# Optimization experiments

Hardware: AMD Instinct MI355X
Metric: run time of the kernel (lower is better)

The kernel has to match this reference:

```python
import jax, jax.numpy as jnp
import numpy as np

BATCH, IN_F, OUT_F = 4096, 1024, 1024


def setup_inputs() -> dict:
    key = jax.random.key(0)
    kx, kw = jax.random.split(key)
    x = jax.random.normal(kx, (BATCH, IN_F, 4), dtype=jnp.float32)
    weight = jax.random.normal(kw, (OUT_F, IN_F, 4), dtype=jnp.float32) * 0.01
    bias = jnp.zeros((OUT_F, 4), dtype=jnp.float32)
    return {"x": x, "weight": weight, "bias": bias}


def reference(x, weight, bias):
    # x: (batch, in, 4) quaternions; weight: (out, in, 4); bias: (out, 4)
    # Hamilton product broadcast over (batch, out, in) then summed over in ==
    # 16 signed real GEMMs contracting the `in` dimension.
    ar, ai, aj, ak = x[..., 0], x[..., 1], x[..., 2], x[..., 3]          # (b, i)
    br, bi, bj, bk = weight[..., 0], weight[..., 1], weight[..., 2], weight[..., 3]  # (o, i)

    mm = lambda a, w: jnp.einsum('bi,oi->bo', a, w)

    out_r = mm(ar, br) - mm(ai, bi) - mm(aj, bj) - mm(ak, bk)
    out_i = mm(ar, bi) + mm(ai, br) + mm(aj, bk) - mm(ak, bj)
    out_j = mm(ar, bj) - mm(ai, bk) + mm(aj, br) + mm(ak, bi)
    out_k = mm(ar, bk) + mm(ai, bj) - mm(aj, bi) + mm(ak, br)

    out = jnp.stack([out_r, out_i, out_j, out_k], axis=-1)  # (b, o, 4)
    return out + bias
```

## Files before the change

### kernel.cpp

```cpp
#include <hip/hip_runtime.h>


typedef __bf16 bf16x8 __attribute__((ext_vector_type(8)));
typedef float floatx4 __attribute__((ext_vector_type(4)));

constexpr int M = 4096;
constexpr int N = 4096;
constexpr int K = 4096;
constexpr int BM = 256, BN = 256, BK = 64;

constexpr int CVT_BLOCKS = (M * K / 8) / 256;
constexpr int EXP_BLOCKS = (1024 * 1024 / 2) / 256;

#define BARRIER() asm volatile("s_barrier" ::: "memory")
#define SB()      __builtin_amdgcn_sched_barrier(0)
#define LGKM0()   do { asm volatile("s_waitcnt lgkmcnt(0)"); SB(); } while (0)
#define LGKM4()   do { asm volatile("s_waitcnt lgkmcnt(4)"); SB(); } while (0)
#define LDS_OFF(p) ((unsigned)(uintptr_t)(__attribute__((address_space(3))) const void*)(p))

__global__ void prep_kernel(const float* __restrict__ x, const float* __restrict__ w,
                            __bf16* __restrict__ A, __bf16* __restrict__ Wb) {
    const int b = blockIdx.x;
    if (b < CVT_BLOCKS) {
        const size_t i = (size_t)b * 256 + threadIdx.x;
        const float4* xp = (const float4*)x;
        float4 a = xp[2 * i];
        float4 c = xp[2 * i + 1];
        bf16x8 v;
        v[0] = (__bf16)a.x; v[1] = (__bf16)a.y; v[2] = (__bf16)a.z; v[3] = (__bf16)a.w;
        v[4] = (__bf16)c.x; v[5] = (__bf16)c.y; v[6] = (__bf16)c.z; v[7] = (__bf16)c.w;
        *(bf16x8*)(A + 8 * i) = v;
    } else {
        const int idx = (b - CVT_BLOCKS) * 256 + threadIdx.x;
        const int o  = idx >> 9;
        const int ip = (idx & 511) * 2;
        float4 q0 = ((const float4*)w)[o * 1024 + ip];
        float4 q1 = ((const float4*)w)[o * 1024 + ip + 1];
        __bf16* base = Wb + (size_t)(o * 4) * K + ip * 4;
        bf16x8 r;
        r[0] = (__bf16)q0.x; r[1] = (__bf16)(-q0.y); r[2] = (__bf16)(-q0.z); r[3] = (__bf16)(-q0.w);
        r[4] = (__bf16)q1.x; r[5] = (__bf16)(-q1.y); r[6] = (__bf16)(-q1.z); r[7] = (__bf16)(-q1.w);
        *(bf16x8*)(base) = r;
        r[0] = (__bf16)q0.y; r[1] = (__bf16)q0.x; r[2] = (__bf16)q0.w; r[3] = (__bf16)(-q0.z);
        r[4] = (__bf16)q1.y; r[5] = (__bf16)q1.x; r[6] = (__bf16)q1.w; r[7] = (__bf16)(-q1.z);
        *(bf16x8*)(base + (size_t)K) = r;
        r[0] = (__bf16)q0.z; r[1] = (__bf16)(-q0.w); r[2] = (__bf16)q0.x; r[3] = (__bf16)q0.y;
        r[4] = (__bf16)q1.z; r[5] = (__bf16)(-q1.w); r[6] = (__bf16)q1.x; r[7] = (__bf16)q1.y;
        *(bf16x8*)(base + (size_t)2 * K) = r;
        r[0] = (__bf16)q0.w; r[1] = (__bf16)q0.z; r[2] = (__bf16)(-q0.y); r[3] = (__bf16)q0.x;
        r[4] = (__bf16)q1.w; r[5] = (__bf16)q1.z; r[6] = (__bf16)(-q1.y); r[7] = (__bf16)q1.x;
        *(bf16x8*)(base + (size_t)3 * K) = r;
    }
}

__device__ __forceinline__ void gload_lds16(const __bf16* g, __bf16* l) {
    __builtin_amdgcn_global_load_lds(
        (const __attribute__((address_space(1))) void*)g,
        (__attribute__((address_space(3))) void*)l, 16, 0, 0);
}

template <int OFF>
__device__ __forceinline__ bf16x8 dsrO(unsigned base) {
    bf16x8 r;
    asm volatile("ds_read_b128 %0, %1 offset:%c2" : "=v"(r) : "v"(base), "i"(OFF));
    return r;
}

__global__ __launch_bounds__(512, 2) void qgemm_kernel(const __bf16* __restrict__ A,
                                                       const __bf16* __restrict__ B,
                                                       const float* __restrict__ bias,
                                                       float* __restrict__ C) {
    __shared__ __bf16 As[3][BM][BK];
    __shared__ __bf16 Bs[2][BN][BK];

    const int tid  = threadIdx.x;
    const int wave = tid >> 6;
    const int lane = tid & 63;

    const int bid = blockIdx.x;
    const int xcd = bid & 7;
    const int q   = bid >> 3;
    const int tm  = (xcd >> 2) * 8 + (q & 7);
    const int tn  = (xcd & 3) * 4 + (q >> 3);
    const int bm  = tm * BM;
    const int bn  = tn * BN;

    const int wm = (wave >> 2) * 128;
    const int wn = (wave & 3) * 64;

    const int srow = wave * 16 + (lane >> 3);
    const int schk = ((lane & 7) ^ (lane >> 3)) * 8;
    const __bf16* agA = A + (size_t)(bm + srow) * K + schk;
    const __bf16* agB = B + (size_t)(bn + srow) * K + schk;

    auto issueA = [&](int buf, int h, int t) {
        const __bf16* g = agA + (size_t)h * 128 * K + t * BK;
        gload_lds16(g,                 &As[buf][h * 128 + wave * 16][0]);
        gload_lds16(g + (size_t)8 * K, &As[buf][h * 128 + wave * 16 + 8][0]);
    };
    auto issueB = [&](int buf, int h, int t) {
        const __bf16* g = agB + (size_t)h * 128 * K + t * BK;
        gload_lds16(g,                 &Bs[buf][h * 128 + wave * 16][0]);
        gload_lds16(g + (size_t)8 * K, &Bs[buf][h * 128 + wave * 16 + 8][0]);
    };

    const int fl  = lane & 15;
    const int fq  = lane >> 4;
    const int fx7 = fl & 7;
    const unsigned ebo0 = (unsigned)(((fq)     ^ fx7) * 16);
    const unsigned ebo1 = (unsigned)(((4 + fq) ^ fx7) * 16);
    const unsigned aR0  = LDS_OFF(&As[0][0][0]) + (unsigned)(wm + fl) * 128u + ebo0;
    const unsigned aR1  = LDS_OFF(&As[0][0][0]) + (unsigned)(wm + fl) * 128u + ebo1;
    const unsigned aR0b1 = aR0 + 32768u, aR1b1 = aR1 + 32768u;
    const unsigned aR0b2 = aR0 + 65536u, aR1b2 = aR1 + 65536u;
    const unsigned bR0  = LDS_OFF(&Bs[0][0][0]) + (unsigned)(wn + fl) * 128u + ebo0;
    const unsigned bR1  = LDS_OFF(&Bs[0][0][0]) + (unsigned)(wn + fl) * 128u + ebo1;
    const unsigned bR0b1 = bR0 + 32768u, bR1b1 = bR1 + 32768u;

    floatx4 acc[8][4] = {};
    bf16x8 x0, x1, x2, x3;
    bf16x8 y0, y1, y2, y3;
    bf16x8 w0, w1, w2, w3;
    bf16x8 z0, z1, z2, z3;
    bf16x8 s0, s1, s2, s3;
    bf16x8 c0, c1, c2, c3;
    bf16x8 d0, d1, d2, d3;
    bf16x8 n0, n1, n2, n3;

#define HALFK(i0, i1, AA, AB, F0, F1, F2, F3)                                     \
    acc[i0][0] = __builtin_amdgcn_mfma_f32_16x16x32_bf16(AA, F0, acc[i0][0], 0, 0, 0); \
    acc[i1][0] = __builtin_amdgcn_mfma_f32_16x16x32_bf16(AB, F0, acc[i1][0], 0, 0, 0); \
    acc[i0][1] = __builtin_amdgcn_mfma_f32_16x16x32_bf16(AA, F1, acc[i0][1], 0, 0, 0); \
    acc[i1][1] = __builtin_amdgcn_mfma_f32_16x16x32_bf16(AB, F1, acc[i1][1], 0, 0, 0); \
    acc[i0][2] = __builtin_amdgcn_mfma_f32_16x16x32_bf16(AA, F2, acc[i0][2], 0, 0, 0); \
    acc[i1][2] = __builtin_amdgcn_mfma_f32_16x16x32_bf16(AB, F2, acc[i1][2], 0, 0, 0); \
    acc[i0][3] = __builtin_amdgcn_mfma_f32_16x16x32_bf16(AA, F3, acc[i0][3], 0, 0, 0); \
    acc[i1][3] = __builtin_amdgcn_mfma_f32_16x16x32_bf16(AB, F3, acc[i1][3], 0, 0, 0)

#define TILE(T, A0c, A1c, A0n, A1n, B0c, B1c, B0x, DA, DB, ISSA, ISSB, MIDVM)     \
    do {                                                                          \
                      \
        if (ISSA) { issueA(DA, 0, (T) + 2); issueA(DA, 1, (T) + 2); }             \
        s0 = dsrO<0>(B1c); s1 = dsrO<2048>(B1c);                                  \
        s2 = dsrO<4096>(B1c); s3 = dsrO<6144>(B1c);                               \
        y0 = dsrO<4096>(A0c); y1 = dsrO<4096>(A1c);                               \
        y2 = dsrO<6144>(A0c); y3 = dsrO<6144>(A1c);                               \
        SB();                                                                     \
        __builtin_amdgcn_s_setprio(1);                                            \
        HALFK(0, 1, x0, x2, c0, c1, c2, c3);                                      \
        __builtin_amdgcn_s_setprio(0);                                            \
        LGKM4();                                       \
        __builtin_amdgcn_s_setprio(1);                                            \
        HALFK(0, 1, x1, x3, s0, s1, s2, s3);                                      \
        __builtin_amdgcn_s_setprio(0);                                            \
                     \
        w0 = dsrO<8192>(A0c); w1 = dsrO<8192>(A1c);                               \
        w2 = dsrO<10240>(A0c); w3 = dsrO<10240>(A1c);                             \
        SB();                                                                     \
        LGKM4();                                       \
        __builtin_amdgcn_s_setprio(1);                                            \
        HALFK(2, 3, y0, y2, c0, c1, c2, c3);                                      \
        HALFK(2, 3, y1, y3, s0, s1, s2, s3);                                      \
        __builtin_amdgcn_s_setprio(0);                                            \
        LGKM0();                                                      \
        asm volatile("s_waitcnt vmcnt(" #MIDVM ")");    \
        BARRIER();                                        \
        if (ISSB) { issueB(DB, 0, (T) + 2); issueB(DB, 1, (T) + 2); }             \
              \
        z0 = dsrO<12288>(A0c); z1 = dsrO<12288>(A1c);                             \
        z2 = dsrO<14336>(A0c); z3 = dsrO<14336>(A1c);                             \
        d0 = dsrO<0>(B0x); d1 = dsrO<2048>(B0x);                                  \
        d2 = dsrO<4096>(B0x); d3 = dsrO<6144>(B0x);                               \
        SB();                                                                     \
        __builtin_amdgcn_s_setprio(1);                                            \
        HALFK(4, 5, w0, w2, c0, c1, c2, c3);                                      \
        HALFK(4, 5, w1, w3, s0, s1, s2, s3);                                      \
        __builtin_amdgcn_s_setprio(0);                                            \
                                        \
        LGKM4();                                       \
        n0 = dsrO<0>(A0n); n1 = dsrO<0>(A1n);                                     \
        n2 = dsrO<2048>(A0n); n3 = dsrO<2048>(A1n);                               \
        SB();                                                                     \
        __builtin_amdgcn_s_setprio(1);                                            \
        HALFK(6, 7, z0, z2, c0, c1, c2, c3);                                      \
        HALFK(6, 7, z1, z3, s0, s1, s2, s3);                                      \
        __builtin_amdgcn_s_setprio(0);                                            \
        LGKM0();                          \
        BARRIER();                                               \
        x0 = n0; x1 = n1; x2 = n2; x3 = n3;                                       \
        c0 = d0; c1 = d1; c2 = d2; c3 = d3;                                       \
    } while (0)

    issueB(0, 0, 0); issueB(0, 1, 0);
    issueA(0, 0, 0); issueA(0, 1, 0);
    issueB(1, 0, 1); issueB(1, 1, 1);
    issueA(1, 0, 1); issueA(1, 1, 1);
    asm volatile("s_waitcnt vmcnt(0)");
    BARRIER();
    x0 = dsrO<0>(aR0);    x1 = dsrO<0>(aR1);
    x2 = dsrO<2048>(aR0); x3 = dsrO<2048>(aR1);
    c0 = dsrO<0>(bR0);    c1 = dsrO<2048>(bR0);
    c2 = dsrO<4096>(bR0); c3 = dsrO<6144>(bR0);
    LGKM0();

    for (int t = 0; t < 60; t += 6) {
        TILE(t + 0, aR0,   aR1,   aR0b1, aR1b1, bR0,   bR1,   bR0b1, 2, 0, true, true, 4);
        TILE(t + 1, aR0b1, aR1b1, aR0b2, aR1b2, bR0b1, bR1b1, bR0,   0, 1, true, true, 4);
        TILE(t + 2, aR0b2, aR1b2, aR0,   aR1,   bR0,   bR1,   bR0b1, 1, 0, true, true, 4);
        TILE(t + 3, aR0,   aR1,   aR0b1, aR1b1, bR0b1, bR1b1, bR0,   2, 1, true, true, 4);
        TILE(t + 4, aR0b1, aR1b1, aR0b2, aR1b2, bR0,   bR1,   bR0b1, 0, 0, true, true, 4);
        TILE(t + 5, aR0b2, aR1b2, aR0,   aR1,   bR0b1, bR1b1, bR0,   1, 1, true, true, 4);
    }
    TILE(60, aR0,   aR1,   aR0b1, aR1b1, bR0,   bR1,   bR0b1, 2, 0, true,  true,  4);
    TILE(61, aR0b1, aR1b1, aR0b2, aR1b2, bR0b1, bR1b1, bR0,   0, 1, true,  true,  4);
    TILE(62, aR0b2, aR1b2, aR0,   aR1,   bR0,   bR1,   bR0b1, 1, 0, false, false, 0);

    {
        s0 = dsrO<0>(bR1b1); s1 = dsrO<2048>(bR1b1);
        s2 = dsrO<4096>(bR1b1); s3 = dsrO<6144>(bR1b1);
        y0 = dsrO<4096>(aR0); y1 = dsrO<4096>(aR1);
        y2 = dsrO<6144>(aR0); y3 = dsrO<6144>(aR1);
        SB();
        __builtin_amdgcn_s_setprio(1);
        HALFK(0, 1, x0, x2, c0, c1, c2, c3);
        __builtin_amdgcn_s_setprio(0);
        LGKM4();
        __builtin_amdgcn_s_setprio(1);
        HALFK(0, 1, x1, x3, s0, s1, s2, s3);
        __builtin_amdgcn_s_setprio(0);
        w0 = dsrO<8192>(aR0); w1 = dsrO<8192>(aR1);
        w2 = dsrO<10240>(aR0); w3 = dsrO<10240>(aR1);
        SB();
        LGKM4();
        __builtin_amdgcn_s_setprio(1);
        HALFK(2, 3, y0, y2, c0, c1, c2, c3);
        HALFK(2, 3, y1, y3, s0, s1, s2, s3);
        __builtin_amdgcn_s_setprio(0);
        LGKM0();
        z0 = dsrO<12288>(aR0); z1 = dsrO<12288>(aR1);
        z2 = dsrO<14336>(aR0); z3 = dsrO<14336>(aR1);
        SB();
        __builtin_amdgcn_s_setprio(1);
        HALFK(4, 5, w0, w2, c0, c1, c2, c3);
        HALFK(4, 5, w1, w3, s0, s1, s2, s3);
        __builtin_amdgcn_s_setprio(0);
        LGKM0();
        __builtin_amdgcn_s_setprio(1);
        HALFK(6, 7, z0, z2, c0, c1, c2, c3);
        HALFK(6, 7, z1, z3, s0, s1, s2, s3);
        __builtin_amdgcn_s_setprio(0);
    }

#pragma unroll
    for (int mt = 0; mt < 8; ++mt) {
        const int row = bm + wm + mt * 16 + fq * 4;
#pragma unroll
        for (int nt = 0; nt < 4; ++nt) {
            const int col = bn + wn + nt * 16 + fl;
            const float bv = bias[col];
            float* cp = C + (size_t)row * N + col;
#pragma unroll
            for (int r = 0; r < 4; ++r)
                cp[(size_t)r * N] = acc[mt][nt][r] + bv;
        }
    }
#undef TILE
#undef HALFK
}

extern "C" void kernel_launch(void* const* d_in, const int* in_sizes, int n_in,
                              void* d_out, int out_size, void* d_ws, size_t ws_size,
                              hipStream_t stream) {
    const float* x    = (const float*)d_in[0];
    const float* w    = (const float*)d_in[1];
    const float* bias = (const float*)d_in[2];
    float* out = (float*)d_out;

    __bf16* Abf  = (__bf16*)d_ws;
    __bf16* Wbig = (__bf16*)((char*)d_ws + (size_t)M * K * 2);

    prep_kernel<<<CVT_BLOCKS + EXP_BLOCKS, 256, 0, stream>>>(x, w, Abf, Wbig);

    qgemm_kernel<<<256, 512, 0, stream>>>(Abf, Wbig, bias, out);
}
```

Before: 235.9 us.

## Fuse fp32-to-bf16 conversion of x into GEMM A-tile loading

The separate pass that converted x (64 MB fp32) to a bf16 buffer is removed. The GEMM now loads fp32 x with global_load_dwordx4 into registers, converts to bf16 and writes swizzled tiles to LDS with ds_write, interleaved into the existing pipeline. B fragments are also double-buffered in named registers instead of being copied at the end of each tile. This removes a 64 MB read plus 32 MB write and the reread of the bf16 A. In exchange the main loop gets more VGPR pressure, extra VALU conversion work and vmcnt waits that may stall the MFMA pipeline.

```diff
diff --git a/kernel.cpp b/kernel.cpp
--- a/kernel.cpp
+++ b/kernel.cpp
@@ -9,48 +9,36 @@
 constexpr int K = 4096;
 constexpr int BM = 256, BN = 256, BK = 64;
 
-constexpr int CVT_BLOCKS = (M * K / 8) / 256;
 constexpr int EXP_BLOCKS = (1024 * 1024 / 2) / 256;
 
 #define BARRIER() asm volatile("s_barrier" ::: "memory")
 #define SB()      __builtin_amdgcn_sched_barrier(0)
 #define LGKM0()   do { asm volatile("s_waitcnt lgkmcnt(0)"); SB(); } while (0)
 #define LGKM4()   do { asm volatile("s_waitcnt lgkmcnt(4)"); SB(); } while (0)
+#define LGKM8()   do { asm volatile("s_waitcnt lgkmcnt(8)"); SB(); } while (0)
+#define VM(n)     do { asm volatile("s_waitcnt vmcnt(" #n ")"); SB(); } while (0)
 #define LDS_OFF(p) ((unsigned)(uintptr_t)(__attribute__((address_space(3))) const void*)(p))
 
-__global__ void prep_kernel(const float* __restrict__ x, const float* __restrict__ w,
-                            __bf16* __restrict__ A, __bf16* __restrict__ Wb) {
-    const int b = blockIdx.x;
-    if (b < CVT_BLOCKS) {
-        const size_t i = (size_t)b * 256 + threadIdx.x;
-        const float4* xp = (const float4*)x;
-        float4 a = xp[2 * i];
-        float4 c = xp[2 * i + 1];
-        bf16x8 v;
-        v[0] = (__bf16)a.x; v[1] = (__bf16)a.y; v[2] = (__bf16)a.z; v[3] = (__bf16)a.w;
-        v[4] = (__bf16)c.x; v[5] = (__bf16)c.y; v[6] = (__bf16)c.z; v[7] = (__bf16)c.w;
-        *(bf16x8*)(A + 8 * i) = v;
-    } else {
-        const int idx = (b - CVT_BLOCKS) * 256 + threadIdx.x;
-        const int o  = idx >> 9;
-        const int ip = (idx & 511) * 2;
-        float4 q0 = ((const float4*)w)[o * 1024 + ip];
-        float4 q1 = ((const float4*)w)[o * 1024 + ip + 1];
-        __bf16* base = Wb + (size_t)(o * 4) * K + ip * 4;
-        bf16x8 r;
-        r[0] = (__bf16)q0.x; r[1] = (__bf16)(-q0.y); r[2] = (__bf16)(-q0.z); r[3] = (__bf16)(-q0.w);
-        r[4] = (__bf16)q1.x; r[5] = (__bf16)(-q1.y); r[6] = (__bf16)(-q1.z); r[7] = (__bf16)(-q1.w);
-        *(bf16x8*)(base) = r;
-        r[0] = (__bf16)q0.y; r[1] = (__bf16)q0.x; r[2] = (__bf16)q0.w; r[3] = (__bf16)(-q0.z);
-        r[4] = (__bf16)q1.y; r[5] = (__bf16)q1.x; r[6] = (__bf16)q1.w; r[7] = (__bf16)(-q1.z);
-        *(bf16x8*)(base + (size_t)K) = r;
-        r[0] = (__bf16)q0.z; r[1] = (__bf16)(-q0.w); r[2] = (__bf16)q0.x; r[3] = (__bf16)q0.y;
-        r[4] = (__bf16)q1.z; r[5] = (__bf16)(-q1.w); r[6] = (__bf16)q1.x; r[7] = (__bf16)q1.y;
-        *(bf16x8*)(base + (size_t)2 * K) = r;
-        r[0] = (__bf16)q0.w; r[1] = (__bf16)q0.z; r[2] = (__bf16)(-q0.y); r[3] = (__bf16)q0.x;
-        r[4] = (__bf16)q1.w; r[5] = (__bf16)q1.z; r[6] = (__bf16)(-q1.y); r[7] = (__bf16)q1.x;
-        *(bf16x8*)(base + (size_t)3 * K) = r;
-    }
+__global__ void prep_kernel(const float* __restrict__ w, __bf16* __restrict__ Wb) {
+    const int idx = blockIdx.x * 256 + threadIdx.x;
+    const int o  = idx >> 9;
+    const int ip = (idx & 511) * 2;
+    float4 q0 = ((const float4*)w)[o * 1024 + ip];
+    float4 q1 = ((const float4*)w)[o * 1024 + ip + 1];
+    __bf16* base = Wb + (size_t)(o * 4) * K + ip * 4;
+    bf16x8 r;
+    r[0] = (__bf16)q0.x; r[1] = (__bf16)(-q0.y); r[2] = (__bf16)(-q0.z); r[3] = (__bf16)(-q0.w);
+    r[4] = (__bf16)q1.x; r[5] = (__bf16)(-q1.y); r[6] = (__bf16)(-q1.z); r[7] = (__bf16)(-q1.w);
+    *(bf16x8*)(base) = r;
+    r[0] = (__bf16)q0.y; r[1] = (__bf16)q0.x; r[2] = (__bf16)q0.w; r[3] = (__bf16)(-q0.z);
+    r[4] = (__bf16)q1.y; r[5] = (__bf16)q1.x; r[6] = (__bf16)q1.w; r[7] = (__bf16)(-q1.z);
+    *(bf16x8*)(base + (size_t)K) = r;
+    r[0] = (__bf16)q0.z; r[1] = (__bf16)(-q0.w); r[2] = (__bf16)q0.x; r[3] = (__bf16)q0.y;
+    r[4] = (__bf16)q1.z; r[5] = (__bf16)(-q1.w); r[6] = (__bf16)q1.x; r[7] = (__bf16)q1.y;
+    *(bf16x8*)(base + (size_t)2 * K) = r;
+    r[0] = (__bf16)q0.w; r[1] = (__bf16)q0.z; r[2] = (__bf16)(-q0.y); r[3] = (__bf16)q0.x;
+    r[4] = (__bf16)q1.w; r[5] = (__bf16)q1.z; r[6] = (__bf16)(-q1.y); r[7] = (__bf16)q1.x;
+    *(bf16x8*)(base + (size_t)3 * K) = r;
 }
 
 __device__ __forceinline__ void gload_lds16(const __bf16* g, __bf16* l) {
@@ -59,14 +47,29 @@
         (__attribute__((address_space(3))) void*)l, 16, 0, 0);
 }
 
+__device__ __forceinline__ float4 gl4(const float* p) {
+    float4 r;
+    asm volatile("global_load_dwordx4 %0, %1, off" : "=v"(r) : "v"(p));
+    return r;
+}
 template <int OFF>
 __device__ __forceinline__ bf16x8 dsrO(unsigned base) {
     bf16x8 r;
     asm volatile("ds_read_b128 %0, %1 offset:%c2" : "=v"(r) : "v"(base), "i"(OFF));
     return r;
 }
-
-__global__ __launch_bounds__(512, 2) void qgemm_kernel(const __bf16* __restrict__ A,
+template <int OFF>
+__device__ __forceinline__ void dswO(unsigned base, bf16x8 v) {
+    asm volatile("ds_write_b128 %0, %1 offset:%c2" :: "v"(base), "v"(v), "i"(OFF));
+}
+__device__ __forceinline__ bf16x8 cvt8(float4 a, float4 b) {
+    bf16x8 v;
+    v[0] = (__bf16)a.x; v[1] = (__bf16)a.y; v[2] = (__bf16)a.z; v[3] = (__bf16)a.w;
+    v[4] = (__bf16)b.x; v[5] = (__bf16)b.y; v[6] = (__bf16)b.z; v[7] = (__bf16)b.w;
+    return v;
+}
+
+__global__ __launch_bounds__(512, 2) void qgemm_kernel(const float* __restrict__ X,
                                                        const __bf16* __restrict__ B,
                                                        const float* __restrict__ bias,
                                                        float* __restrict__ C) {
@@ -88,21 +91,20 @@
     const int wm = (wave >> 2) * 128;
     const int wn = (wave & 3) * 64;
 
+    const float* agX = X + (size_t)(bm + wave * 16 + (lane >> 3)) * 4096 + (lane & 7) * 8;
     const int srow = wave * 16 + (lane >> 3);
     const int schk = ((lane & 7) ^ (lane >> 3)) * 8;
-    const __bf16* agA = A + (size_t)(bm + srow) * K + schk;
     const __bf16* agB = B + (size_t)(bn + srow) * K + schk;
 
-    auto issueA = [&](int buf, int h, int t) {
-        const __bf16* g = agA + (size_t)h * 128 * K + t * BK;
-        gload_lds16(g,                 &As[buf][h * 128 + wave * 16][0]);
-        gload_lds16(g + (size_t)8 * K, &As[buf][h * 128 + wave * 16 + 8][0]);
-    };
     auto issueB = [&](int buf, int h, int t) {
         const __bf16* g = agB + (size_t)h * 128 * K + t * BK;
         gload_lds16(g,                 &Bs[buf][h * 128 + wave * 16][0]);
         gload_lds16(g + (size_t)8 * K, &Bs[buf][h * 128 + wave * 16 + 8][0]);
     };
+
+    const unsigned aW0 = LDS_OFF(&As[0][0][0]) + (unsigned)((wave * 16 + (lane >> 3)) * 128)
+                       + (unsigned)(((lane & 7) ^ (lane >> 3)) * 16);
+    const unsigned aW1 = aW0 + 32768u, aW2 = aW0 + 65536u;
 
     const int fl  = lane & 15;
     const int fq  = lane >> 4;
@@ -118,14 +120,12 @@
     const unsigned bR0b1 = bR0 + 32768u, bR1b1 = bR1 + 32768u;
 
     floatx4 acc[8][4] = {};
-    bf16x8 x0, x1, x2, x3;
-    bf16x8 y0, y1, y2, y3;
-    bf16x8 w0, w1, w2, w3;
-    bf16x8 z0, z1, z2, z3;
+    bf16x8 xa0, xa1, xa2, xa3;
+    bf16x8 xb0, xb1, xb2, xb3;
     bf16x8 s0, s1, s2, s3;
-    bf16x8 c0, c1, c2, c3;
-    bf16x8 d0, d1, d2, d3;
-    bf16x8 n0, n1, n2, n3;
+    bf16x8 bE0, bE1, bE2, bE3;
+    bf16x8 bO0, bO1, bO2, bO3;
+    float4 fa0, fa1, fa2, fa3;
 
 #define HALFK(i0, i1, AA, AB, F0, F1, F2, F3)                                     \
     acc[i0][0] = __builtin_amdgcn_mfma_f32_16x16x32_bf16(AA, F0, acc[i0][0], 0, 0, 0); \
@@ -137,117 +137,161 @@
     acc[i0][3] = __builtin_amdgcn_mfma_f32_16x16x32_bf16(AA, F3, acc[i0][3], 0, 0, 0); \
     acc[i1][3] = __builtin_amdgcn_mfma_f32_16x16x32_bf16(AB, F3, acc[i1][3], 0, 0, 0)
 
-#define TILE(T, A0c, A1c, A0n, A1n, B0c, B1c, B0x, DA, DB, ISSA, ISSB, MIDVM)     \
+#define TILE(T, A0c, A1c, A0n, A1n, B0c, B1c, B0x, AW, BC0, BC1, BC2, BC3,        \
+             BX0, BX1, BX2, BX3, DB, ISSA, ISSB, MIDVM)                           \
     do {                                                                          \
-                      \
-        if (ISSA) { issueA(DA, 0, (T) + 2); issueA(DA, 1, (T) + 2); }             \
+                                                                          \
+        if (ISSA) {                                                               \
+            const float* g_ = agX + (size_t)((T) + 2) * 64;                       \
+            fa0 = gl4(g_);          fa1 = gl4(g_ + 4);                            \
+            fa2 = gl4(g_ + 32768);  fa3 = gl4(g_ + 32772);                        \
+        }                                                                         \
         s0 = dsrO<0>(B1c); s1 = dsrO<2048>(B1c);                                  \
         s2 = dsrO<4096>(B1c); s3 = dsrO<6144>(B1c);                               \
-        y0 = dsrO<4096>(A0c); y1 = dsrO<4096>(A1c);                               \
-        y2 = dsrO<6144>(A0c); y3 = dsrO<6144>(A1c);                               \
+        xb0 = dsrO<4096>(A0c); xb1 = dsrO<4096>(A1c);                             \
+        xb2 = dsrO<6144>(A0c); xb3 = dsrO<6144>(A1c);                             \
         SB();                                                                     \
         __builtin_amdgcn_s_setprio(1);                                            \
-        HALFK(0, 1, x0, x2, c0, c1, c2, c3);                                      \
-        __builtin_amdgcn_s_setprio(0);                                            \
-        LGKM4();                                       \
-        __builtin_amdgcn_s_setprio(1);                                            \
-        HALFK(0, 1, x1, x3, s0, s1, s2, s3);                                      \
-        __builtin_amdgcn_s_setprio(0);                                            \
-                     \
-        w0 = dsrO<8192>(A0c); w1 = dsrO<8192>(A1c);                               \
-        w2 = dsrO<10240>(A0c); w3 = dsrO<10240>(A1c);                             \
+        HALFK(0, 1, xa0, xa2, BC0, BC1, BC2, BC3);                                \
+        __builtin_amdgcn_s_setprio(0);                                            \
+        LGKM4();                                                                  \
+        __builtin_amdgcn_s_setprio(1);                                            \
+        HALFK(0, 1, xa1, xa3, s0, s1, s2, s3);                                    \
+        __builtin_amdgcn_s_setprio(0);                                            \
+                                                                          \
+        xa0 = dsrO<8192>(A0c); xa1 = dsrO<8192>(A1c);                             \
+        xa2 = dsrO<10240>(A0c); xa3 = dsrO<10240>(A1c);                           \
         SB();                                                                     \
-        LGKM4();                                       \
-        __builtin_amdgcn_s_setprio(1);                                            \
-        HALFK(2, 3, y0, y2, c0, c1, c2, c3);                                      \
-        HALFK(2, 3, y1, y3, s0, s1, s2, s3);                                      \
-        __builtin_amdgcn_s_setprio(0);                                            \
-        LGKM0();                                                      \
-        asm volatile("s_waitcnt vmcnt(" #MIDVM ")");    \
-        BARRIER();                                        \
+        LGKM4();                                                                  \
+        __builtin_amdgcn_s_setprio(1);                                            \
+        HALFK(2, 3, xb0, xb2, BC0, BC1, BC2, BC3);                                \
+        HALFK(2, 3, xb1, xb3, s0, s1, s2, s3);                                    \
+        __builtin_amdgcn_s_setprio(0);                                            \
+        LGKM0();                                                                  \
+        asm volatile("s_waitcnt vmcnt(" #MIDVM ")");                              \
+        BARRIER();                                                                \
+                                                                          \
+        if (ISSA) {                                                               \
+            VM(0);                           \
+            dswO<0>(AW, cvt8(fa0, fa1));                                          \
+            dswO<1024>(AW, cvt8(fa2, fa3));                                       \
+            const float* g_ = agX + (size_t)((T) + 2) * 64 + 524288;              \
+            fa0 = gl4(g_);          fa1 = gl4(g_ + 4);                            \
+            fa2 = gl4(g_ + 32768);  fa3 = gl4(g_ + 32772);                        \
+        }                                                                         \
         if (ISSB) { issueB(DB, 0, (T) + 2); issueB(DB, 1, (T) + 2); }             \
-              \
-        z0 = dsrO<12288>(A0c); z1 = dsrO<12288>(A1c);                             \
-        z2 = dsrO<14336>(A0c); z3 = dsrO<14336>(A1c);                             \
-        d0 = dsrO<0>(B0x); d1 = dsrO<2048>(B0x);                                  \
-        d2 = dsrO<4096>(B0x); d3 = dsrO<6144>(B0x);                               \
+        xb0 = dsrO<12288>(A0c); xb1 = dsrO<12288>(A1c);                           \
+        xb2 = dsrO<14336>(A0c); xb3 = dsrO<14336>(A1c);                           \
+        BX0 = dsrO<0>(B0x); BX1 = dsrO<2048>(B0x);                                \
+        BX2 = dsrO<4096>(B0x); BX3 = dsrO<6144>(B0x);                             \
         SB();                                                                     \
         __builtin_amdgcn_s_setprio(1);                                            \
-        HALFK(4, 5, w0, w2, c0, c1, c2, c3);                                      \
-        HALFK(4, 5, w1, w3, s0, s1, s2, s3);                                      \
-        __builtin_amdgcn_s_setprio(0);                                            \
-                                        \
-        LGKM4();                                       \
-        n0 = dsrO<0>(A0n); n1 = dsrO<0>(A1n);                                     \
-        n2 = dsrO<2048>(A0n); n3 = dsrO<2048>(A1n);                               \
+        HALFK(4, 5, xa0, xa2, BC0, BC1, BC2, BC3);                                \
+        HALFK(4, 5, xa1, xa3, s0, s1, s2, s3);                                    \
+        __builtin_amdgcn_s_setprio(0);                                            \
+                                                                          \
+        xa0 = dsrO<0>(A0n); xa1 = dsrO<0>(A1n);                                   \
+        xa2 = dsrO<2048>(A0n); xa3 = dsrO<2048>(A1n);                             \
         SB();                                                                     \
-        __builtin_amdgcn_s_setprio(1);                                            \
-        HALFK(6, 7, z0, z2, c0, c1, c2, c3);                                      \
-        HALFK(6, 7, z1, z3, s0, s1, s2, s3);                                      \
-        __builtin_amdgcn_s_setprio(0);                                            \
-        LGKM0();                          \
-        BARRIER();                                               \
-        x0 = n0; x1 = n1; x2 = n2; x3 = n3;                                       \
-        c0 = d0; c1 = d1; c2 = d2; c3 = d3;                                       \
+        LGKM8();                                     \
+        __builtin_amdgcn_s_setprio(1);                                            \
+        HALFK(6, 7, xb0, xb2, BC0, BC1, BC2, BC3);                                \
+        __builtin_amdgcn_s_setprio(0);                                            \
+        if (ISSA) {                                                               \
+            VM(4);                         \
+            dswO<16384>(AW, cvt8(fa0, fa1));                                      \
+            dswO<17408>(AW, cvt8(fa2, fa3));                                      \
+        }                                                                         \
+        __builtin_amdgcn_s_setprio(1);                                            \
+        HALFK(6, 7, xb1, xb3, s0, s1, s2, s3);                                    \
+        __builtin_amdgcn_s_setprio(0);                                            \
+        LGKM0();                                                                  \
+        BARRIER();                                                                \
     } while (0)
 
+    {
+        const float* g_ = agX;
+        fa0 = gl4(g_); fa1 = gl4(g_ + 4); fa2 = gl4(g_ + 32768); fa3 = gl4(g_ + 32772);
+        VM(0);
+        dswO<0>(aW0, cvt8(fa0, fa1)); dswO<1024>(aW0, cvt8(fa2, fa3));
+        g_ = agX + 524288;
+        fa0 = gl4(g_); fa1 = gl4(g_ + 4); fa2 = gl4(g_ + 32768); fa3 = gl4(g_ + 32772);
+        VM(0);
+        dswO<16384>(aW0, cvt8(fa0, fa1)); dswO<17408>(aW0, cvt8(fa2, fa3));
+        g_ = agX + 64;
+        fa0 = gl4(g_); fa1 = gl4(g_ + 4); fa2 = gl4(g_ + 32768); fa3 = gl4(g_ + 32772);
+        VM(0);
+        dswO<0>(aW1, cvt8(fa0, fa1)); dswO<1024>(aW1, cvt8(fa2, fa3));
+        g_ = agX + 64 + 524288;
+        fa0 = gl4(g_); fa1 = gl4(g_ + 4); fa2 = gl4(g_ + 32768); fa3 = gl4(g_ + 32772);
+        VM(0);
+        dswO<16384>(aW1, cvt8(fa0, fa1)); dswO<17408>(aW1, cvt8(fa2, fa3));
+    }
     issueB(0, 0, 0); issueB(0, 1, 0);
-    issueA(0, 0, 0); issueA(0, 1, 0);
     issueB(1, 0, 1); issueB(1, 1, 1);
-    issueA(1, 0, 1); issueA(1, 1, 1);
-    asm volatile("s_waitcnt vmcnt(0)");
+    VM(4);
+    LGKM0();
     BARRIER();
-    x0 = dsrO<0>(aR0);    x1 = dsrO<0>(aR1);
-    x2 = dsrO<2048>(aR0); x3 = dsrO<2048>(aR1);
-    c0 = dsrO<0>(bR0);    c1 = dsrO<2048>(bR0);
-    c2 = dsrO<4096>(bR0); c3 = dsrO<6144>(bR0);
+    xa0 = dsrO<0>(aR0);    xa1 = dsrO<0>(aR1);
+    xa2 = dsrO<2048>(aR0); xa3 = dsrO<2048>(aR1);
+    bE0 = dsrO<0>(bR0);    bE1 = dsrO<2048>(bR0);
+    bE2 = dsrO<4096>(bR0); bE3 = dsrO<6144>(bR0);
     LGKM0();
 
     for (int t = 0; t < 60; t += 6) {
-        TILE(t + 0, aR0,   aR1,   aR0b1, aR1b1, bR0,   bR1,   bR0b1, 2, 0, true, true, 4);
-        TILE(t + 1, aR0b1, aR1b1, aR0b2, aR1b2, bR0b1, bR1b1, bR0,   0, 1, true, true, 4);
-        TILE(t + 2, aR0b2, aR1b2, aR0,   aR1,   bR0,   bR1,   bR0b1, 1, 0, true, true, 4);
-        TILE(t + 3, aR0,   aR1,   aR0b1, aR1b1, bR0b1, bR1b1, bR0,   2, 1, true, true, 4);
-        TILE(t + 4, aR0b1, aR1b1, aR0b2, aR1b2, bR0,   bR1,   bR0b1, 0, 0, true, true, 4);
-        TILE(t + 5, aR0b2, aR1b2, aR0,   aR1,   bR0b1, bR1b1, bR0,   1, 1, true, true, 4);
+        TILE(t + 0, aR0,   aR1,   aR0b1, aR1b1, bR0,   bR1,   bR0b1, aW2,
+             bE0, bE1, bE2, bE3, bO0, bO1, bO2, bO3, 0, true, true, 4);
+        TILE(t + 1, aR0b1, aR1b1, aR0b2, aR1b2, bR0b1, bR1b1, bR0,   aW0,
+             bO0, bO1, bO2, bO3, bE0, bE1, bE2, bE3, 1, true, true, 4);
+        TILE(t + 2, aR0b2, aR1b2, aR0,   aR1,   bR0,   bR1,   bR0b1, aW1,
+             bE0, bE1, bE2, bE3, bO0, bO1, bO2, bO3, 0, true, true, 4);
+        TILE(t + 3, aR0,   aR1,   aR0b1, aR1b1, bR0b1, bR1b1, bR0,   aW2,
+             bO0, bO1, bO2, bO3, bE0, bE1, bE2, bE3, 1, true, true, 4);
+        TILE(t + 4, aR0b1, aR1b1, aR0b2, aR1b2, bR0,   bR1,   bR0b1, aW0,
+             bE0, bE1, bE2, bE3, bO0, bO1, bO2, bO3, 0, true, true, 4);
+        TILE(t + 5, aR0b2, aR1b2, aR0,   aR1,   bR0b1, bR1b1, bR0,   aW1,
+             bO0, bO1, bO2, bO3, bE0, bE1, bE2, bE3, 1, true, true, 4);
     }
-    TILE(60, aR0,   aR1,   aR0b1, aR1b1, bR0,   bR1,   bR0b1, 2, 0, true,  true,  4);
-    TILE(61, aR0b1, aR1b1, aR0b2, aR1b2, bR0b1, bR1b1, bR0,   0, 1, true,  true,  4);
-    TILE(62, aR0b2, aR1b2, aR0,   aR1,   bR0,   bR1,   bR0b1, 1, 0, false, false, 0);
+    TILE(60, aR0,   aR1,   aR0b1, aR1b1, bR0,   bR1,   bR0b1, aW2,
+         bE0, bE1, bE2, bE3, bO0, bO1, bO2, bO3, 0, true,  true,  4);
+    TILE(61, aR0b1, aR1b1, aR0b2, aR1b2, bR0b1, bR1b1, bR0,   aW0,
+         bO0, bO1, bO2, bO3, bE0, bE1, bE2, bE3, 1, true,  true,  4);
+    TILE(62, aR0b2, aR1b2, aR0,   aR1,   bR0,   bR1,   bR0b1, aW1,
+         bE0, bE1, bE2, bE3, bO0, bO1, bO2, bO3, 0, false, false, 0);
 
     {
         s0 = dsrO<0>(bR1b1); s1 = dsrO<2048>(bR1b1);
         s2 = dsrO<4096>(bR1b1); s3 = dsrO<6144>(bR1b1);
-        y0 = dsrO<4096>(aR0); y1 = dsrO<4096>(aR1);
-        y2 = dsrO<6144>(aR0); y3 = dsrO<6144>(aR1);
+        xb0 = dsrO<4096>(aR0); xb1 = dsrO<4096>(aR1);
+        xb2 = dsrO<6144>(aR0); xb3 = dsrO<6144>(aR1);
         SB();
         __builtin_amdgcn_s_setprio(1);
-        HALFK(0, 1, x0, x2, c0, c1, c2, c3);
+        HALFK(0, 1, xa0, xa2, bO0, bO1, bO2, bO3);
         __builtin_amdgcn_s_setprio(0);
         LGKM4();
         __builtin_amdgcn_s_setprio(1);
-        HALFK(0, 1, x1, x3, s0, s1, s2, s3);
-        __builtin_amdgcn_s_setprio(0);
-        w0 = dsrO<8192>(aR0); w1 = dsrO<8192>(aR1);
-        w2 = dsrO<10240>(aR0); w3 = dsrO<10240>(aR1);
+        HALFK(0, 1, xa1, xa3, s0, s1, s2, s3);
+        __builtin_amdgcn_s_setprio(0);
+        xa0 = dsrO<8192>(aR0); xa1 = dsrO<8192>(aR1);
+        xa2 = dsrO<10240>(aR0); xa3 = dsrO<10240>(aR1);
         SB();
         LGKM4();
         __builtin_amdgcn_s_setprio(1);
-        HALFK(2, 3, y0, y2, c0, c1, c2, c3);
-        HALFK(2, 3, y1, y3, s0, s1, s2, s3);
+        HALFK(2, 3, xb0, xb2, bO0, bO1, bO2, bO3);
+        HALFK(2, 3, xb1, xb3, s0, s1, s2, s3);
         __builtin_amdgcn_s_setprio(0);
         LGKM0();
-        z0 = dsrO<12288>(aR0); z1 = dsrO<12288>(aR1);
-        z2 = dsrO<14336>(aR0); z3 = dsrO<14336>(aR1);
+        xb0 = dsrO<12288>(aR0); xb1 = dsrO<12288>(aR1);
+        xb2 = dsrO<14336>(aR0); xb3 = dsrO<14336>(aR1);
         SB();
         __builtin_amdgcn_s_setprio(1);
-        HALFK(4, 5, w0, w2, c0, c1, c2, c3);
-        HALFK(4, 5, w1, w3, s0, s1, s2, s3);
+        HALFK(4, 5, xa0, xa2, bO0, bO1, bO2, bO3);
+        HALFK(4, 5, xa1, xa3, s0, s1, s2, s3);
         __builtin_amdgcn_s_setprio(0);
         LGKM0();
         __builtin_amdgcn_s_setprio(1);
-        HALFK(6, 7, z0, z2, c0, c1, c2, c3);
-        HALFK(6, 7, z1, z3, s0, s1, s2, s3);
+        HALFK(6, 7, xb0, xb2, bO0, bO1, bO2, bO3);
+        HALFK(6, 7, xb1, xb3, s0, s1, s2, s3);
         __builtin_amdgcn_s_setprio(0);
     }
 
@@ -276,10 +320,9 @@
     const float* bias = (const float*)d_in[2];
     float* out = (float*)d_out;
 
-    __bf16* Abf  = (__bf16*)d_ws;
-    __bf16* Wbig = (__bf16*)((char*)d_ws + (size_t)M * K * 2);
-
-    prep_kernel<<<CVT_BLOCKS + EXP_BLOCKS, 256, 0, stream>>>(x, w, Abf, Wbig);
-
-    qgemm_kernel<<<256, 512, 0, stream>>>(Abf, Wbig, bias, out);
-}
+    __bf16* Wbig = (__bf16*)d_ws;
+
+    prep_kernel<<<EXP_BLOCKS, 256, 0, stream>>>(w, Wbig);
+
+    qgemm_kernel<<<256, 512, 0, stream>>>(x, Wbig, bias, out);
+}
```

Measured after the change: 256.7 us. +8.8%, slower.
